# Kernel tuning notes

Measured on AMD Instinct MI355X. Metric: run time of the kernel, lower is better.

The kernel has to match this reference:

```python
import jax, jax.numpy as jnp
import numpy as np
import math

EMBED_DIM = 256
NUM_HEADS = 8
SEQ_LEN = 6
HEAD_DIM = EMBED_DIM // NUM_HEADS


def setup_inputs() -> dict:
    key = jax.random.key(0)
    ks = jax.random.split(key, 10)
    B, S, E, H, W = 16, SEQ_LEN, EMBED_DIM, 64, 64
    s = 1.0 / math.sqrt(E)
    return {
        "frame_features": jax.random.normal(ks[0], (B, S, E, H, W), dtype=jnp.float32),
        "Wq": jax.random.uniform(ks[1], (E, E), jnp.float32, -s, s),
        "bq": jnp.zeros((E,), jnp.float32),
        "Wk": jax.random.uniform(ks[2], (E, E), jnp.float32, -s, s),
        "bk": jnp.zeros((E,), jnp.float32),
        "Wv": jax.random.uniform(ks[3], (E, E), jnp.float32, -s, s),
        "bv": jnp.zeros((E,), jnp.float32),
        "Wo": jax.random.uniform(ks[4], (E, E), jnp.float32, -s, s),
        "bo": jnp.zeros((E,), jnp.float32),
        "temporal_pos": jax.random.normal(ks[5], (S, E), dtype=jnp.float32),
    }


def reference(frame_features, Wq, bq, Wk, bk, Wv, bv, Wo, bo, temporal_pos):
    B, S, E, H, W = frame_features.shape
    scale = math.sqrt(HEAD_DIM)
    # adaptive_avg_pool2d to (1,1) == global spatial mean
    g = frame_features.mean(axis=(-2, -1)) + temporal_pos[None]  # [B,S,E]
    q = g @ Wq.T + bq
    k = g @ Wk.T + bk
    v = g @ Wv.T + bv
    # [B,h,S,d]
    def split_heads(x):
        return x.reshape(B, S, NUM_HEADS, HEAD_DIM).transpose(0, 2, 1, 3)
    q, k, v = split_heads(q), split_heads(k), split_heads(v)
    scores = jnp.einsum('bhsd,bhtd->bhst', q, k) / scale
    causal = jnp.triu(jnp.ones((S, S), dtype=bool), k=1)
    scores = jnp.where(causal[None, None], -jnp.inf, scores)
    attn = jax.nn.softmax(scores, axis=-1)  # dropout is identity in eval
    attended = jnp.einsum('bhst,bhtd->bhsd', attn, v)
    attended = attended.transpose(0, 2, 1, 3).reshape(B, S, E)
    out_g = attended @ Wo.T + bo  # [B,S,E]
    cross = frame_features + out_g[:, :, :, None, None]
    return cross, attn
```

## Files before the change

kernel.cpp:

```cpp
#include <hip/hip_runtime.h>
#include <math.h>

#define B_ 16
#define S_ 6
#define E_ 256
#define NH_ 8
#define HD_ 32
#define HW_ 4096
#define ROWS_ (B_*S_*E_)
#define SE_ (S_*E_)
#define CROSS_N_ ((size_t)ROWS_*HW_)
#define TRB_ 64

typedef float f4_t __attribute__((ext_vector_type(4)));

__global__ __launch_bounds__(256) void pool_tr_kernel(
    const float* __restrict__ ff, const float* __restrict__ tpos,
    float* __restrict__ g,
    const float* __restrict__ Wq, const float* __restrict__ Wk,
    const float* __restrict__ Wv, const float* __restrict__ Wo,
    float* __restrict__ WT)
{
    if (blockIdx.x < ROWS_) {
        const int row = blockIdx.x;
        const f4_t* p = (const f4_t*)(ff + (size_t)row * HW_);
        float sum = 0.f;
        #pragma unroll
        for (int i = 0; i < 4; ++i) {
            f4_t v = p[threadIdx.x + i * 256];
            sum += v.x + v.y + v.z + v.w;
        }
        #pragma unroll
        for (int off = 32; off > 0; off >>= 1)
            sum += __shfl_down(sum, off, 64);
        __shared__ float part[4];
        if ((threadIdx.x & 63) == 0) part[threadIdx.x >> 6] = sum;
        __syncthreads();
        if (threadIdx.x == 0) {
            float tot = part[0] + part[1] + part[2] + part[3];
            g[row] = tot * (1.0f / HW_) + tpos[row % SE_];
        }
    } else {
        __shared__ float tile[64][65];
        const int tb = blockIdx.x - ROWS_;
        const int m  = tb >> 4;
        const int t  = tb & 15;
        const int tr = t >> 2, tc = t & 3;
        const float* W = (m == 0) ? Wq : (m == 1) ? Wk : (m == 2) ? Wv : Wo;
        float* out = WT + (size_t)m * E_ * E_;
        const int c  = threadIdx.x & 63;
        const int r0 = threadIdx.x >> 6;
        #pragma unroll
        for (int k = 0; k < 16; ++k) {
            int r = k * 4 + r0;
            tile[r][c] = W[(size_t)(tr * 64 + r) * E_ + tc * 64 + c];
        }
        __syncthreads();
        #pragma unroll
        for (int k = 0; k < 16; ++k) {
            int r = k * 4 + r0;
            out[(size_t)(tc * 64 + r) * E_ + tr * 64 + c] = tile[c][r];
        }
    }
}

__global__ __launch_bounds__(256) void attn_kernel(
    const float* __restrict__ g, const float* __restrict__ WT,
    const float* __restrict__ bq, const float* __restrict__ bk,
    const float* __restrict__ bv, const float* __restrict__ bo,
    float* __restrict__ out_g, float* __restrict__ attn_out)
{
    __shared__ float sg[S_][E_], sq[S_][E_], sk[S_][E_], sv[S_][E_], satd[S_][E_];
    __shared__ float satt[NH_][S_][S_];
    const int b = blockIdx.x;
    const int e = threadIdx.x;
    const float* WqT = WT;
    const float* WkT = WT + E_ * E_;
    const float* WvT = WT + 2 * E_ * E_;
    const float* WoT = WT + 3 * E_ * E_;

    #pragma unroll
    for (int s = 0; s < S_; ++s)
        sg[s][e] = g[(size_t)b * SE_ + s * E_ + e];
    __syncthreads();

    {
        float aq[S_], ak[S_], av[S_];
        #pragma unroll
        for (int s = 0; s < S_; ++s) { aq[s] = bq[e]; ak[s] = bk[e]; av[s] = bv[e]; }
        #pragma unroll 4
        for (int i = 0; i < E_; ++i) {
            float wq = WqT[i * E_ + e];
            float wk = WkT[i * E_ + e];
            float wv = WvT[i * E_ + e];
            #pragma unroll
            for (int s = 0; s < S_; ++s) {
                float gv = sg[s][i];
                aq[s] = fmaf(gv, wq, aq[s]);
                ak[s] = fmaf(gv, wk, ak[s]);
                av[s] = fmaf(gv, wv, av[s]);
            }
        }
        #pragma unroll
        for (int s = 0; s < S_; ++s) {
            sq[s][e] = aq[s]; sk[s][e] = ak[s]; sv[s][e] = av[s];
        }
    }
    __syncthreads();

    const float inv_scale = rsqrtf((float)HD_);
    for (int idx = e; idx < NH_ * S_ * S_; idx += 256) {
        int h = idx / (S_ * S_);
        int r = idx % (S_ * S_);
        int s = r / S_, t = r % S_;
        float sc = -INFINITY;
        if (t <= s) {
            sc = 0.f;
            #pragma unroll
            for (int d = 0; d < HD_; ++d)
                sc = fmaf(sq[s][h * HD_ + d], sk[t][h * HD_ + d], sc);
            sc *= inv_scale;
        }
        satt[h][s][t] = sc;
    }
    __syncthreads();

    if (e < NH_ * S_) {
        int h = e / S_, s = e % S_;
        float m = -INFINITY;
        #pragma unroll
        for (int t = 0; t < S_; ++t)
            if (t <= s) m = fmaxf(m, satt[h][s][t]);
        float ex[S_], sum = 0.f;
        #pragma unroll
        for (int t = 0; t < S_; ++t) {
            ex[t] = (t <= s) ? expf(satt[h][s][t] - m) : 0.0f;
            sum += ex[t];
        }
        float inv = 1.0f / sum;
        #pragma unroll
        for (int t = 0; t < S_; ++t)
            satt[h][s][t] = ex[t] * inv;
    }
    __syncthreads();

    {
        const int h = e >> 5;
        #pragma unroll
        for (int s = 0; s < S_; ++s) {
            float a = 0.f;
            #pragma unroll
            for (int t = 0; t < S_; ++t)
                if (t <= s) a = fmaf(satt[h][s][t], sv[t][e], a);
            satd[s][e] = a;
        }
    }
    __syncthreads();

    {
        float ao[S_];
        #pragma unroll
        for (int s = 0; s < S_; ++s) ao[s] = bo[e];
        #pragma unroll 4
        for (int i = 0; i < E_; ++i) {
            float wo = WoT[i * E_ + e];
            #pragma unroll
            for (int s = 0; s < S_; ++s)
                ao[s] = fmaf(satd[s][i], wo, ao[s]);
        }
        #pragma unroll
        for (int s = 0; s < S_; ++s)
            out_g[(size_t)b * SE_ + s * E_ + e] = ao[s];
    }

    for (int idx = e; idx < NH_ * S_ * S_; idx += 256) {
        int h = idx / (S_ * S_);
        int r = idx % (S_ * S_);
        attn_out[(size_t)b * (NH_ * S_ * S_) + idx] = satt[h][r / S_][r % S_];
    }
}

__global__ __launch_bounds__(256) void add_kernel(
    const float* __restrict__ ff, const float* __restrict__ out_g,
    float* __restrict__ cross)
{
    const int row = (ROWS_ - 1) - blockIdx.x;
    const float add = out_g[row];
    const f4_t* p = (const f4_t*)(ff + (size_t)row * HW_);
    f4_t* q = (f4_t*)(cross + (size_t)row * HW_);
    #pragma unroll
    for (int i = 0; i < 4; ++i) {
        f4_t v = __builtin_nontemporal_load(&p[threadIdx.x + i * 256]);
        v += add;
        __builtin_nontemporal_store(v, &q[threadIdx.x + i * 256]);
    }
}

extern "C" void kernel_launch(void* const* d_in, const int* in_sizes, int n_in,
                              void* d_out, int out_size, void* d_ws, size_t ws_size,
                              hipStream_t stream) {
    const float* ff   = (const float*)d_in[0];
    const float* Wq   = (const float*)d_in[1];
    const float* bq   = (const float*)d_in[2];
    const float* Wk   = (const float*)d_in[3];
    const float* bk   = (const float*)d_in[4];
    const float* Wv   = (const float*)d_in[5];
    const float* bv   = (const float*)d_in[6];
    const float* Wo   = (const float*)d_in[7];
    const float* bo   = (const float*)d_in[8];
    const float* tpos = (const float*)d_in[9];

    float* out   = (float*)d_out;
    float* g     = (float*)d_ws;
    float* out_g = g + ROWS_;
    float* WT    = out_g + ROWS_;

    float* cross    = out;
    float* attn_out = out + CROSS_N_;

    pool_tr_kernel<<<ROWS_ + TRB_, 256, 0, stream>>>(ff, tpos, g, Wq, Wk, Wv, Wo, WT);
    attn_kernel<<<B_, 256, 0, stream>>>(g, WT, bq, bk, bv, bo, out_g, attn_out);
    add_kernel<<<ROWS_, 256, 0, stream>>>(ff, out_g, cross);
}
```

Baseline: 745.2 us.

## Split attention kernel into QKV, core, and out-projection kernels for more blocks

Splits the single 16-block attention kernel into three kernels. The QKV and output projections now run over 96 blocks, one per (batch, seq) row, and the attention core keeps one block per batch. This raises parallelism for the projection GEMVs, which were serialized on only 16 CUs, at the cost of extra launches, workspace round-trips and repeated weight reads per row. The add kernel's input load also changes from nontemporal to a normal load.

```diff
diff --git a/kernel.cpp b/kernel.cpp
--- a/kernel.cpp
+++ b/kernel.cpp
@@ -8,6 +8,7 @@
 #define HD_ 32
 #define HW_ 4096
 #define ROWS_ (B_*S_*E_)
+#define BS_ (B_*S_)
 #define SE_ (S_*E_)
 #define CROSS_N_ ((size_t)ROWS_*HW_)
 #define TRB_ 64
@@ -64,47 +65,50 @@
     }
 }
 
-__global__ __launch_bounds__(256) void attn_kernel(
+__global__ __launch_bounds__(256) void qkv_kernel(
     const float* __restrict__ g, const float* __restrict__ WT,
     const float* __restrict__ bq, const float* __restrict__ bk,
-    const float* __restrict__ bv, const float* __restrict__ bo,
-    float* __restrict__ out_g, float* __restrict__ attn_out)
-{
-    __shared__ float sg[S_][E_], sq[S_][E_], sk[S_][E_], sv[S_][E_], satd[S_][E_];
+    const float* __restrict__ bv,
+    float* __restrict__ qws, float* __restrict__ kws, float* __restrict__ vws)
+{
+    __shared__ float sg[E_];
+    const int bs = blockIdx.x;
+    const int e  = threadIdx.x;
+    const float* WqT = WT;
+    const float* WkT = WT + E_ * E_;
+    const float* WvT = WT + 2 * E_ * E_;
+
+    sg[e] = g[(size_t)bs * E_ + e];
+    __syncthreads();
+
+    float aq = bq[e], ak = bk[e], av = bv[e];
+    #pragma unroll 8
+    for (int i = 0; i < E_; ++i) {
+        float gv = sg[i];
+        aq = fmaf(gv, WqT[i * E_ + e], aq);
+        ak = fmaf(gv, WkT[i * E_ + e], ak);
+        av = fmaf(gv, WvT[i * E_ + e], av);
+    }
+    qws[(size_t)bs * E_ + e] = aq;
+    kws[(size_t)bs * E_ + e] = ak;
+    vws[(size_t)bs * E_ + e] = av;
+}
+
+__global__ __launch_bounds__(256) void core_kernel(
+    const float* __restrict__ qws, const float* __restrict__ kws,
+    const float* __restrict__ vws,
+    float* __restrict__ satd_ws, float* __restrict__ attn_out)
+{
+    __shared__ float sq[S_][E_], sk[S_][E_], sv[S_][E_];
     __shared__ float satt[NH_][S_][S_];
     const int b = blockIdx.x;
     const int e = threadIdx.x;
-    const float* WqT = WT;
-    const float* WkT = WT + E_ * E_;
-    const float* WvT = WT + 2 * E_ * E_;
-    const float* WoT = WT + 3 * E_ * E_;
 
     #pragma unroll
-    for (int s = 0; s < S_; ++s)
-        sg[s][e] = g[(size_t)b * SE_ + s * E_ + e];
-    __syncthreads();
-
-    {
-        float aq[S_], ak[S_], av[S_];
-        #pragma unroll
-        for (int s = 0; s < S_; ++s) { aq[s] = bq[e]; ak[s] = bk[e]; av[s] = bv[e]; }
-        #pragma unroll 4
-        for (int i = 0; i < E_; ++i) {
-            float wq = WqT[i * E_ + e];
-            float wk = WkT[i * E_ + e];
-            float wv = WvT[i * E_ + e];
-            #pragma unroll
-            for (int s = 0; s < S_; ++s) {
-                float gv = sg[s][i];
-                aq[s] = fmaf(gv, wq, aq[s]);
-                ak[s] = fmaf(gv, wk, ak[s]);
-                av[s] = fmaf(gv, wv, av[s]);
-            }
-        }
-        #pragma unroll
-        for (int s = 0; s < S_; ++s) {
-            sq[s][e] = aq[s]; sk[s][e] = ak[s]; sv[s][e] = av[s];
-        }
+    for (int s = 0; s < S_; ++s) {
+        sq[s][e] = qws[(size_t)b * SE_ + s * E_ + e];
+        sk[s][e] = kws[(size_t)b * SE_ + s * E_ + e];
+        sv[s][e] = vws[(size_t)b * SE_ + s * E_ + e];
     }
     __syncthreads();
 
@@ -152,25 +156,8 @@
             #pragma unroll
             for (int t = 0; t < S_; ++t)
                 if (t <= s) a = fmaf(satt[h][s][t], sv[t][e], a);
-            satd[s][e] = a;
-        }
-    }
-    __syncthreads();
-
-    {
-        float ao[S_];
-        #pragma unroll
-        for (int s = 0; s < S_; ++s) ao[s] = bo[e];
-        #pragma unroll 4
-        for (int i = 0; i < E_; ++i) {
-            float wo = WoT[i * E_ + e];
-            #pragma unroll
-            for (int s = 0; s < S_; ++s)
-                ao[s] = fmaf(satd[s][i], wo, ao[s]);
-        }
-        #pragma unroll
-        for (int s = 0; s < S_; ++s)
-            out_g[(size_t)b * SE_ + s * E_ + e] = ao[s];
+            satd_ws[(size_t)b * SE_ + s * E_ + e] = a;
+        }
     }
 
     for (int idx = e; idx < NH_ * S_ * S_; idx += 256) {
@@ -178,6 +165,25 @@
         int r = idx % (S_ * S_);
         attn_out[(size_t)b * (NH_ * S_ * S_) + idx] = satt[h][r / S_][r % S_];
     }
+}
+
+__global__ __launch_bounds__(256) void outproj_kernel(
+    const float* __restrict__ satd_ws, const float* __restrict__ WT,
+    const float* __restrict__ bo, float* __restrict__ out_g)
+{
+    __shared__ float sa[E_];
+    const int bs = blockIdx.x;
+    const int e  = threadIdx.x;
+    const float* WoT = WT + 3 * E_ * E_;
+
+    sa[e] = satd_ws[(size_t)bs * E_ + e];
+    __syncthreads();
+
+    float ao = bo[e];
+    #pragma unroll 8
+    for (int i = 0; i < E_; ++i)
+        ao = fmaf(sa[i], WoT[i * E_ + e], ao);
+    out_g[(size_t)bs * E_ + e] = ao;
 }
 
 __global__ __launch_bounds__(256) void add_kernel(
@@ -190,7 +196,7 @@
     f4_t* q = (f4_t*)(cross + (size_t)row * HW_);
     #pragma unroll
     for (int i = 0; i < 4; ++i) {
-        f4_t v = __builtin_nontemporal_load(&p[threadIdx.x + i * 256]);
+        f4_t v = p[threadIdx.x + i * 256];
         v += add;
         __builtin_nontemporal_store(v, &q[threadIdx.x + i * 256]);
     }
@@ -214,11 +220,17 @@
     float* g     = (float*)d_ws;
     float* out_g = g + ROWS_;
     float* WT    = out_g + ROWS_;
+    float* qws   = WT + 4 * E_ * E_;
+    float* kws   = qws + ROWS_;
+    float* vws   = kws + ROWS_;
+    float* satd  = vws + ROWS_;
 
     float* cross    = out;
     float* attn_out = out + CROSS_N_;
 
     pool_tr_kernel<<<ROWS_ + TRB_, 256, 0, stream>>>(ff, tpos, g, Wq, Wk, Wv, Wo, WT);
-    attn_kernel<<<B_, 256, 0, stream>>>(g, WT, bq, bk, bv, bo, out_g, attn_out);
+    qkv_kernel<<<BS_, 256, 0, stream>>>(g, WT, bq, bk, bv, qws, kws, vws);
+    core_kernel<<<B_, 256, 0, stream>>>(qws, kws, vws, satd, attn_out);
+    outproj_kernel<<<BS_, 256, 0, stream>>>(satd, WT, bo, out_g);
     add_kernel<<<ROWS_, 256, 0, stream>>>(ff, out_g, cross);
 }
```

After: 732.8 us. No clear change (-1.7%).
